# Optimization experiments

Hardware: AMD Instinct MI355X
Metric: run time of the kernel (lower is better)

Reference implementation:

```python
import jax, jax.numpy as jnp
import numpy as np

N = 100000   # nodes
E = 1600000  # edges (avg degree 16)
IN = 24
HID = 128
OUT = 12


def setup_inputs() -> dict:
    key = jax.random.key(0)
    ks = jax.random.split(key, 16)
    s = 0.05
    return {
        "inputs": jax.random.normal(ks[0], (N, IN), jnp.float32),
        "src": jax.random.randint(ks[1], (E,), 0, N),
        "dst": jax.random.randint(ks[2], (E,), 0, N),
        "e_w": jax.random.uniform(ks[3], (E, 1), jnp.float32),
        "snorm_n": jax.random.uniform(ks[4], (N, 1), jnp.float32),
        "snorm_e": jax.random.uniform(ks[5], (E, 1), jnp.float32),
        "W_emb": jax.random.normal(ks[6], (IN, HID), jnp.float32) * s,
        "b_emb": jnp.zeros((HID,), jnp.float32),
        "W_self1": jax.random.normal(ks[7], (HID, HID), jnp.float32) * s,
        "W1": jax.random.normal(ks[8], (HID, HID), jnp.float32) * s,
        "b1": jnp.zeros((HID,), jnp.float32),
        "W_self2": jax.random.normal(ks[9], (HID, HID), jnp.float32) * s,
        "W2": jax.random.normal(ks[10], (HID, HID), jnp.float32) * s,
        "b2": jnp.zeros((HID,), jnp.float32),
        "W_fc": jax.random.normal(ks[11], (HID, OUT), jnp.float32) * s,
        "b_fc": jnp.zeros((OUT,), jnp.float32),
    }


def _degrees(src, dst):
    out_deg = jnp.clip(jnp.zeros((N,), jnp.float32).at[src].add(1.0), 1.0)
    in_deg = jnp.clip(jnp.zeros((N,), jnp.float32).at[dst].add(1.0), 1.0)
    return out_deg, in_deg


def _gcn_layer(h, src, dst, e_w, out_deg, in_deg, W_self, W, b):
    # self transform (no bias)
    h_s = h @ W_self
    # source-side symmetric norm, edge-weighted message, sum-aggregate at dst
    feat = h * (out_deg ** -0.5)[:, None]          # [N, H]
    m = feat[src] * e_w                            # [E, H]  u_mul_e
    agg = jax.ops.segment_sum(m, dst, num_segments=N)  # [N, H] sum reduce
    h2 = (agg @ W + b) * (in_deg ** -0.5)[:, None]
    return h_s + h2


def reference(inputs, src, dst, e_w, snorm_n, snorm_e,
              W_emb, b_emb, W_self1, W1, b1, W_self2, W2, b2, W_fc, b_fc):
    out_deg, in_deg = _degrees(src, dst)
    h = inputs @ W_emb + b_emb
    h = jax.nn.relu(_gcn_layer(h, src, dst, e_w, out_deg, in_deg, W_self1, W1, b1))
    h = jax.nn.relu(_gcn_layer(h, src, dst, e_w, out_deg, in_deg, W_self2, W2, b2))
    return h @ W_fc + b_fc
```

## Files before the change

### kernel.cpp

```cpp
#include <hip/hip_runtime.h>

#define NN 100000
#define EE 1600000
#define IN_F 24
#define HID 128
#define OUT_F 12
#define HC 256
#define LBLK 128

#define DEG_WIN 16384
#define DEG_GRP 7
#define DEG_BPG 48
#define DEG_BLKS (DEG_GRP * DEG_BPG)

#define NBKT 782
#define PA_BLKS 512
#define PA_EPB 3125

#define EMB_B 2048
#define PREP_B 264
#define K1_GRID (DEG_BLKS + PA_BLKS + EMB_B + PREP_B)

typedef unsigned char u8;
typedef unsigned short u16;
typedef unsigned int u32;

using short8 = __attribute__((ext_vector_type(8))) short;
using f32x4  = __attribute__((ext_vector_type(4))) float;

__device__ __forceinline__ float bf2f(u16 h) {
  return __uint_as_float(((u32)h) << 16);
}
__device__ __forceinline__ u16 f2bf(float f) {
  u32 u = __float_as_uint(f);
  u32 r = (u + 0x7FFFu + ((u >> 16) & 1u)) >> 16;
  return (u16)r;
}
__device__ __forceinline__ float inv_sqrt_cnt(int c) {
  if (c < 1) c = 1;
  return 1.0f / sqrtf((float)c);
}

__device__ __forceinline__ void emb_body(int eb, const float* __restrict__ inputs,
                                         const float* __restrict__ W_emb,
                                         const float* __restrict__ b_emb,
                                         u16* __restrict__ hcat, float* smemW) {
  int t = threadIdx.x;
  float* Wls = smemW;
  float* bls = smemW + IN_F * HID;
  for (int i = t; i < IN_F * HID; i += 256) Wls[i] = W_emb[i];
  if (t < HID) bls[t] = b_emb[t];
  __syncthreads();
  int c = t & 127;
  int sub = t >> 7;
  for (int node = eb * 2 + sub; node < NN; node += EMB_B * 2) {
    const float* xr = inputs + (size_t)node * IN_F;
    float acc = bls[c];
    #pragma unroll
    for (int k = 0; k < IN_F; ++k) acc = fmaf(xr[k], Wls[k * HID + c], acc);
    hcat[(size_t)node * HC + c] = f2bf(acc);
  }
}

__device__ __forceinline__ void prep_body(int pb,
    const float* __restrict__ Ws1, const float* __restrict__ W1m,
    const float* __restrict__ Ws2, const float* __restrict__ W2m,
    const float* __restrict__ Wfc,
    u16* __restrict__ WT1, u16* __restrict__ WT2, u16* __restrict__ WfcT) {
  int idx = pb * 256 + (int)threadIdx.x;
  if (idx < 65536) {
    int layer = idx >> 15;
    int rem = idx & 32767;
    int n = rem >> 8, k = rem & 255;
    const float* A = layer ? Ws2 : Ws1;
    const float* B = layer ? W2m : W1m;
    float v = (k < HID) ? A[(size_t)k * HID + n] : B[(size_t)(k - HID) * HID + n];
    (layer ? WT2 : WT1)[(size_t)n * 256 + k] = f2bf(v);
  } else if (idx < 65536 + 2048) {
    int j = idx - 65536;
    int n = j >> 7, k = j & 127;
    WfcT[(size_t)n * 128 + k] = f2bf(n < OUT_F ? Wfc[(size_t)k * OUT_F + n] : 0.f);
  }
}

__global__ __launch_bounds__(256) void k1(
    const int* __restrict__ src, const int* __restrict__ dst,
    u16* __restrict__ whist, u32* __restrict__ histg,
    const float* __restrict__ inputs, const float* __restrict__ W_emb,
    const float* __restrict__ b_emb, u16* __restrict__ hcat,
    const float* __restrict__ Ws1, const float* __restrict__ W1m,
    const float* __restrict__ Ws2, const float* __restrict__ W2m,
    const float* __restrict__ Wfc,
    u16* __restrict__ WT1, u16* __restrict__ WT2, u16* __restrict__ WfcT) {
  __shared__ __align__(16) char sm_raw[65536];
  int b = blockIdx.x, t = threadIdx.x;
  if (b < DEG_BLKS) {
    u32* hist = (u32*)sm_raw;
    int g = b / DEG_BPG, sb = b % DEG_BPG;
    for (int i = t; i < DEG_WIN; i += 256) hist[i] = 0;
    __syncthreads();
    for (int e = sb * 256 + t; e < EE; e += DEG_BPG * 256) {
      int s = src[e];
      if ((s >> 14) == g) atomicAdd(&hist[s & (DEG_WIN - 1)], 1u);
    }
    __syncthreads();
    u16* wout = whist + (size_t)b * DEG_WIN;
    for (int i = t; i < DEG_WIN; i += 256) wout[i] = (u16)hist[i];
  } else if (b < DEG_BLKS + PA_BLKS) {
    u32* hist = (u32*)sm_raw;
    int pb = b - DEG_BLKS;
    for (int i = t; i < 1024; i += 256) hist[i] = 0;
    __syncthreads();
    int e0 = pb * PA_EPB;
    for (int e = e0 + t; e < e0 + PA_EPB; e += 256)
      atomicAdd(&hist[dst[e] >> 7], 1u);
    __syncthreads();
    for (int i = t; i < 1024; i += 256) histg[(size_t)pb * 1024 + i] = hist[i];
  } else if (b < DEG_BLKS + PA_BLKS + EMB_B) {
    emb_body(b - DEG_BLKS - PA_BLKS, inputs, W_emb, b_emb, hcat, (float*)sm_raw);
  } else {
    prep_body(b - DEG_BLKS - PA_BLKS - EMB_B, Ws1, W1m, Ws2, W2m, Wfc, WT1, WT2, WfcT);
  }
}

__global__ __launch_bounds__(256) void k2scan1(const u16* __restrict__ whist,
                                               float* __restrict__ out_norm,
                                               u32* __restrict__ histg,
                                               u32* __restrict__ totals) {
  __shared__ u32 s[512];
  int b = blockIdx.x, t = threadIdx.x;
  if (b < NBKT) {
    int k = b;
    u32 v0 = histg[(size_t)t * 1024 + k];
    u32 v1 = histg[(size_t)(t + 256) * 1024 + k];
    s[t] = v0; s[t + 256] = v1;
    __syncthreads();
    for (int off = 1; off < 512; off <<= 1) {
      u32 a0 = (t >= off) ? s[t - off] : 0;
      u32 a1 = (t + 256 >= off) ? s[t + 256 - off] : 0;
      __syncthreads();
      s[t] += a0; s[t + 256] += a1;
      __syncthreads();
    }
    histg[(size_t)t * 1024 + k] = s[t] - v0;
    histg[(size_t)(t + 256) * 1024 + k] = s[t + 256] - v1;
    if (t == 255) totals[k] = s[511];
  } else {
    int n = (b - NBKT) * 256 + t;
    if (n < NN) {
      int g = n >> 14, i = n & (DEG_WIN - 1);
      const u16* base = whist + ((size_t)g * DEG_BPG) * DEG_WIN + i;
      u32 sum = 0;
      #pragma unroll
      for (int bb = 0; bb < DEG_BPG; ++bb) sum += base[(size_t)bb * DEG_WIN];
      out_norm[n] = inv_sqrt_cnt((int)sum);
    }
  }
}

__global__ __launch_bounds__(1024) void k_scan2(const u32* __restrict__ totals,
                                                u32* __restrict__ estart) {
  __shared__ u32 s[1024];
  int t = threadIdx.x;
  u32 v = (t < NBKT) ? totals[t] : 0;
  s[t] = v;
  __syncthreads();
  for (int off = 1; off < 1024; off <<= 1) {
    u32 a = (t >= off) ? s[t - off] : 0;
    __syncthreads();
    s[t] += a;
    __syncthreads();
  }
  if (t < NBKT) estart[t] = s[t] - v;
  if (t == NBKT - 1) estart[NBKT] = s[t];
}

__global__ __launch_bounds__(256) void k_passb(
    const int* __restrict__ src, const int* __restrict__ dst,
    const float* __restrict__ e_w, const float* __restrict__ out_norm,
    const u32* __restrict__ histg, const u32* __restrict__ estart,
    u32* __restrict__ csr_stage, u8* __restrict__ dl8) {
  __shared__ u32 cur[1024];
  int pb = blockIdx.x, t = threadIdx.x;
  for (int i = t; i < 1024; i += 256)
    cur[i] = ((i < NBKT) ? estart[i] : 0u) + histg[(size_t)pb * 1024 + i];
  __syncthreads();
  int e0 = pb * PA_EPB;
  for (int e = e0 + t; e < e0 + PA_EPB; e += 256) {
    int s = src[e], d = dst[e];
    float w = e_w[e] * out_norm[s];
    u32 pos = atomicAdd(&cur[d >> 7], 1u);
    csr_stage[pos] = (((u32)f2bf(w)) << 17) | (u32)s;
    dl8[pos] = (u8)(d & 127);
  }
}

__global__ __launch_bounds__(256) void k_reorder(
    const u32* __restrict__ csr_stage, const u8* __restrict__ dl8,
    const u32* __restrict__ estart, u32* __restrict__ csr,
    int* __restrict__ row_start, float* __restrict__ in_norm) {
  __shared__ u32 cnt[128], pfx[128], cur[128];
  int k = blockIdx.x, t = threadIdx.x;
  if (t < 128) cnt[t] = 0;
  __syncthreads();
  int e0 = (int)estart[k], e1 = (int)estart[k + 1];
  for (int e = e0 + t; e < e1; e += 256) atomicAdd(&cnt[dl8[e]], 1u);
  __syncthreads();
  if (t < 128) pfx[t] = cnt[t];
  __syncthreads();
  for (int off = 1; off < 128; off <<= 1) {
    u32 v = (t < 128 && t >= off) ? pfx[t - off] : 0;
    __syncthreads();
    if (t < 128) pfx[t] += v;
    __syncthreads();
  }
  if (t < 128) {
    u32 start = (u32)e0 + pfx[t] - cnt[t];
    cur[t] = start;
    int node = k * 128 + t;
    if (node < NN) {
      row_start[node] = (int)start;
      in_norm[node] = inv_sqrt_cnt((int)cnt[t]);
    }
  }
  if (k == NBKT - 1 && t == 0) row_start[NN] = e1;
  __syncthreads();
  for (int e = e0 + t; e < e1; e += 256) {
    u32 pos = atomicAdd(&cur[dl8[e]], 1u);
    csr[pos] = csr_stage[e];
  }
}

__global__ __launch_bounds__(256) void k_agg(const u16* __restrict__ hcat_in,
                                             const int* __restrict__ row_start,
                                             const float* __restrict__ in_norm,
                                             const u32* __restrict__ csr,
                                             u16* __restrict__ hcat_out) {
  int t = threadIdx.x;
  int node = blockIdx.x * 8 + (t >> 5);
  if (node >= NN) return;
  int lane = t & 31;
  int s0 = row_start[node], s1 = row_start[node + 1];
  float ax = 0.f, ay = 0.f, az = 0.f, aw = 0.f;
  for (int i0 = s0; i0 < s1; i0 += 32) {
    u32 pk = 0;
    if (i0 + lane < s1) pk = csr[i0 + lane];
    int m = s1 - i0; if (m > 32) m = 32;
    for (int j = 0; j < m; ++j) {
      u32 p = __shfl(pk, j, 32);
      float w = bf2f((u16)(p >> 17));
      int sv = (int)(p & 0x1FFFF);
      ushort4 hv = *(const ushort4*)(hcat_in + (size_t)sv * HC + lane * 4);
      ax = fmaf(w, bf2f(hv.x), ax);
      ay = fmaf(w, bf2f(hv.y), ay);
      az = fmaf(w, bf2f(hv.z), az);
      aw = fmaf(w, bf2f(hv.w), aw);
    }
  }
  float inn = in_norm[node];
  ushort4 r;
  r.x = f2bf(ax * inn); r.y = f2bf(ay * inn);
  r.z = f2bf(az * inn); r.w = f2bf(aw * inn);
  *(ushort4*)(hcat_out + (size_t)node * HC + HID + lane * 4) = r;
}

template<int FC>
__global__ __launch_bounds__(512) void k_layer(u16* __restrict__ hcat,
    const u16* __restrict__ WT, const float* __restrict__ bias,
    const float* __restrict__ in_norm,
    const u16* __restrict__ WfcT, const float* __restrict__ b_fc,
    float* __restrict__ out) {
  __shared__ char smem[135168];
  const int t = threadIdx.x;
  const int r0 = blockIdx.x * LBLK;

  #pragma unroll
  for (int i = 0; i < 8; ++i) {
    int boff = i * 8192 + t * 16;
    int row = boff >> 9, col = boff & 511;
    uint4 v = *(const uint4*)(hcat + (size_t)(r0 + row) * HC + (col >> 1));
    *(uint4*)(smem + row * 512 + (col ^ ((row & 7) << 4))) = v;
  }
  #pragma unroll
  for (int i = 0; i < 8; ++i) {
    int boff = i * 8192 + t * 16;
    int row = boff >> 9, col = boff & 511;
    uint4 v = *(const uint4*)(WT + (size_t)row * 256 + (col >> 1));
    *(uint4*)(smem + 65536 + row * 512 + (col ^ ((row & 7) << 4))) = v;
  }
  if (FC && t < 256) {
    int row = t >> 4, col = (t & 15) * 16;
    uint4 v = *(const uint4*)(WfcT + (size_t)row * 128 + (col >> 1));
    *(uint4*)(smem + 131072 + row * 256 + (col ^ ((row & 7) << 4))) = v;
  }
  __syncthreads();

  const int lane = t & 63, w = t >> 6;
  const int l15 = lane & 15, lhi = lane >> 4;

  f32x4 acc[8];
  #pragma unroll
  for (int nf = 0; nf < 8; ++nf) acc[nf] = (f32x4){0.f, 0.f, 0.f, 0.f};

  const int arow = w * 16 + l15;
  const char* pa = smem + arow * 512;
  const int aswz = (arow & 7) << 4;
  #pragma unroll
  for (int ks = 0; ks < 8; ++ks) {
    int kb = ks * 64 + (lhi << 4);
    short8 a = *(const short8*)(pa + (kb ^ aswz));
    #pragma unroll
    for (int nf = 0; nf < 8; ++nf) {
      int brow = nf * 16 + l15;
      short8 bf = *(const short8*)(smem + 65536 + brow * 512 + (kb ^ ((brow & 7) << 4)));
      acc[nf] = __builtin_amdgcn_mfma_f32_16x16x32_bf16(a, bf, acc[nf], 0, 0, 0);
    }
  }

  float bcol[8];
  #pragma unroll
  for (int nf = 0; nf < 8; ++nf) bcol[nf] = bias[nf * 16 + l15];

  if (!FC) {
    #pragma unroll
    for (int r = 0; r < 4; ++r) {
      int grow = r0 + w * 16 + (lhi << 2) + r;
      if (grow < NN) {
        float inn = in_norm[grow];
        #pragma unroll
        for (int nf = 0; nf < 8; ++nf) {
          float v = acc[nf][r] + inn * bcol[nf];
          hcat[(size_t)grow * HC + nf * 16 + l15] = f2bf(fmaxf(v, 0.f));
        }
      }
    }
  } else {
    #pragma unroll
    for (int r = 0; r < 4; ++r) {
      int lrow = w * 16 + (lhi << 2) + r;
      int grow = r0 + lrow;
      float inn = (grow < NN) ? in_norm[grow] : 0.f;
      #pragma unroll
      for (int nf = 0; nf < 8; ++nf) {
        int col = nf * 16 + l15;
        float v = fmaxf(acc[nf][r] + inn * bcol[nf], 0.f);
        *(u16*)(smem + lrow * 256 + ((col * 2) ^ ((lrow & 7) << 4))) = f2bf(v);
      }
    }
    __syncthreads();
    f32x4 a2 = (f32x4){0.f, 0.f, 0.f, 0.f};
    const char* pa2 = smem + (w * 16 + l15) * 256;
    const int as2 = (l15 & 7) << 4;
    #pragma unroll
    for (int ks = 0; ks < 4; ++ks) {
      int kb = ks * 64 + (lhi << 4);
      short8 a = *(const short8*)(pa2 + (kb ^ as2));
      short8 bf = *(const short8*)(smem + 131072 + l15 * 256 + (kb ^ as2));
      a2 = __builtin_amdgcn_mfma_f32_16x16x32_bf16(a, bf, a2, 0, 0, 0);
    }
    if (l15 < OUT_F) {
      float bo = b_fc[l15];
      #pragma unroll
      for (int r = 0; r < 4; ++r) {
        int grow = r0 + w * 16 + (lhi << 2) + r;
        if (grow < NN) out[(size_t)grow * OUT_F + l15] = a2[r] + bo;
      }
    }
  }
}

extern "C" void kernel_launch(void* const* d_in, const int* in_sizes, int n_in,
                              void* d_out, int out_size, void* d_ws, size_t ws_size,
                              hipStream_t stream) {
  (void)in_sizes; (void)n_in; (void)out_size;
  const float* inputs  = (const float*)d_in[0];
  const int*   src     = (const int*)d_in[1];
  const int*   dst     = (const int*)d_in[2];
  const float* e_w     = (const float*)d_in[3];
  const float* W_emb   = (const float*)d_in[6];
  const float* b_emb   = (const float*)d_in[7];
  const float* W_self1 = (const float*)d_in[8];
  const float* W1      = (const float*)d_in[9];
  const float* b1      = (const float*)d_in[10];
  const float* W_self2 = (const float*)d_in[11];
  const float* W2      = (const float*)d_in[12];
  const float* b2      = (const float*)d_in[13];
  const float* W_fc    = (const float*)d_in[14];
  const float* b_fc    = (const float*)d_in[15];
  float* out = (float*)d_out;

  u32* histg       = (u32*)d_ws;
  u32* totals      = histg + (size_t)512 * 1024;
  u32* estart      = totals + 1024;
  float* out_norm  = (float*)(estart + 1024);
  float* in_norm   = out_norm + NN;
  int* row_start   = (int*)(in_norm + NN);
  u32* csr_stage   = (u32*)(row_start + NN + 4);
  u8* dl8          = (u8*)(csr_stage + EE);
  u32* csr         = (u32*)(dl8 + EE);
  u16* hcat        = (u16*)(csr + EE);
  u16* WT1         = hcat + (size_t)NN * HC;
  u16* WT2         = WT1 + 32768;
  u16* WfcT        = WT2 + 32768;
  u16* whist       = (u16*)csr_stage;

  const size_t NEED = (size_t)512 * 1024 * 4 + 2048 * 4 + (size_t)(3 * NN + 4) * 4
                      + (size_t)EE * 9 + (size_t)NN * HC * 2 + (2 * 32768 + 2048) * 2;
  if (ws_size < NEED) return;

  hipLaunchKernelGGL(k1, dim3(K1_GRID), dim3(256), 0, stream,
                     src, dst, whist, histg, inputs, W_emb, b_emb, hcat,
                     W_self1, W1, W_self2, W2, W_fc, WT1, WT2, WfcT);
  hipLaunchKernelGGL(k2scan1, dim3(NBKT + (NN + 255) / 256), dim3(256), 0, stream,
                     whist, out_norm, histg, totals);
  hipLaunchKernelGGL(k_scan2, dim3(1), dim3(1024), 0, stream, totals, estart);
  hipLaunchKernelGGL(k_passb, dim3(PA_BLKS), dim3(256), 0, stream,
                     src, dst, e_w, out_norm, histg, estart, csr_stage, dl8);
  hipLaunchKernelGGL(k_reorder, dim3(NBKT), dim3(256), 0, stream,
                     csr_stage, dl8, estart, csr, row_start, in_norm);
  hipLaunchKernelGGL(k_agg, dim3((NN + 7) / 8), dim3(256), 0, stream,
                     hcat, row_start, in_norm, csr, hcat);
  hipLaunchKernelGGL(k_layer<0>, dim3((NN + LBLK - 1) / LBLK), dim3(512), 0, stream,
                     hcat, WT1, b1, in_norm, WfcT, b_fc, out);
  hipLaunchKernelGGL(k_agg, dim3((NN + 7) / 8), dim3(256), 0, stream,
                     hcat, row_start, in_norm, csr, hcat);
  hipLaunchKernelGGL(k_layer<1>, dim3((NN + LBLK - 1) / LBLK), dim3(512), 0, stream,
                     hcat, WT2, b2, in_norm, WfcT, b_fc, out);
}
```

Before: 389.3 us.

## Compute out-degree via bucketed counting sort instead of windowed histograms

Replaces the 336-block windowed shared-memory histogram for source out-degrees, which read the whole src array 48 times per group, with a two-level bucket count. Src is counted alongside dst in k1, scanned, scattered into 128-node buckets of low-byte ids, then counted per bucket to produce out_norm. This cuts redundant src reads and frees 64KB of LDS in k1, at the cost of two extra kernel launches and an extra scatter pass over the edges. The lo8 buffer is reused for dl8 afterwards.

```diff
diff --git a/kernel.cpp b/kernel.cpp
--- a/kernel.cpp
+++ b/kernel.cpp
@@ -8,18 +8,13 @@
 #define HC 256
 #define LBLK 128
 
-#define DEG_WIN 16384
-#define DEG_GRP 7
-#define DEG_BPG 48
-#define DEG_BLKS (DEG_GRP * DEG_BPG)
-
 #define NBKT 782
 #define PA_BLKS 512
 #define PA_EPB 3125
 
 #define EMB_B 2048
 #define PREP_B 264
-#define K1_GRID (DEG_BLKS + PA_BLKS + EMB_B + PREP_B)
+#define K1_GRID (PA_BLKS + EMB_B + PREP_B)
 
 typedef unsigned char u8;
 typedef unsigned short u16;
@@ -85,84 +80,71 @@
 
 __global__ __launch_bounds__(256) void k1(
     const int* __restrict__ src, const int* __restrict__ dst,
-    u16* __restrict__ whist, u32* __restrict__ histg,
+    u32* __restrict__ histgD, u32* __restrict__ histgS,
     const float* __restrict__ inputs, const float* __restrict__ W_emb,
     const float* __restrict__ b_emb, u16* __restrict__ hcat,
     const float* __restrict__ Ws1, const float* __restrict__ W1m,
     const float* __restrict__ Ws2, const float* __restrict__ W2m,
     const float* __restrict__ Wfc,
     u16* __restrict__ WT1, u16* __restrict__ WT2, u16* __restrict__ WfcT) {
-  __shared__ __align__(16) char sm_raw[65536];
+  __shared__ __align__(16) char sm[13312];
   int b = blockIdx.x, t = threadIdx.x;
-  if (b < DEG_BLKS) {
-    u32* hist = (u32*)sm_raw;
-    int g = b / DEG_BPG, sb = b % DEG_BPG;
-    for (int i = t; i < DEG_WIN; i += 256) hist[i] = 0;
-    __syncthreads();
-    for (int e = sb * 256 + t; e < EE; e += DEG_BPG * 256) {
-      int s = src[e];
-      if ((s >> 14) == g) atomicAdd(&hist[s & (DEG_WIN - 1)], 1u);
-    }
-    __syncthreads();
-    u16* wout = whist + (size_t)b * DEG_WIN;
-    for (int i = t; i < DEG_WIN; i += 256) wout[i] = (u16)hist[i];
-  } else if (b < DEG_BLKS + PA_BLKS) {
-    u32* hist = (u32*)sm_raw;
-    int pb = b - DEG_BLKS;
-    for (int i = t; i < 1024; i += 256) hist[i] = 0;
-    __syncthreads();
-    int e0 = pb * PA_EPB;
-    for (int e = e0 + t; e < e0 + PA_EPB; e += 256)
-      atomicAdd(&hist[dst[e] >> 7], 1u);
-    __syncthreads();
-    for (int i = t; i < 1024; i += 256) histg[(size_t)pb * 1024 + i] = hist[i];
-  } else if (b < DEG_BLKS + PA_BLKS + EMB_B) {
-    emb_body(b - DEG_BLKS - PA_BLKS, inputs, W_emb, b_emb, hcat, (float*)sm_raw);
+  if (b < PA_BLKS) {
+    u32* histD = (u32*)sm;
+    u32* histS = histD + 1024;
+    for (int i = t; i < 2048; i += 256) histD[i] = 0;
+    __syncthreads();
+    int e0 = b * PA_EPB;
+    for (int e = e0 + t; e < e0 + PA_EPB; e += 256) {
+      atomicAdd(&histD[dst[e] >> 7], 1u);
+      atomicAdd(&histS[src[e] >> 7], 1u);
+    }
+    __syncthreads();
+    for (int i = t; i < 1024; i += 256) {
+      histgD[(size_t)b * 1024 + i] = histD[i];
+      histgS[(size_t)b * 1024 + i] = histS[i];
+    }
+  } else if (b < PA_BLKS + EMB_B) {
+    emb_body(b - PA_BLKS, inputs, W_emb, b_emb, hcat, (float*)sm);
   } else {
-    prep_body(b - DEG_BLKS - PA_BLKS - EMB_B, Ws1, W1m, Ws2, W2m, Wfc, WT1, WT2, WfcT);
-  }
-}
-
-__global__ __launch_bounds__(256) void k2scan1(const u16* __restrict__ whist,
-                                               float* __restrict__ out_norm,
-                                               u32* __restrict__ histg,
-                                               u32* __restrict__ totals) {
+    prep_body(b - PA_BLKS - EMB_B, Ws1, W1m, Ws2, W2m, Wfc, WT1, WT2, WfcT);
+  }
+}
+
+__global__ __launch_bounds__(256) void k_scan1(u32* __restrict__ histgD,
+                                               u32* __restrict__ histgS,
+                                               u32* __restrict__ totalsD,
+                                               u32* __restrict__ totalsS) {
   __shared__ u32 s[512];
   int b = blockIdx.x, t = threadIdx.x;
-  if (b < NBKT) {
-    int k = b;
-    u32 v0 = histg[(size_t)t * 1024 + k];
-    u32 v1 = histg[(size_t)(t + 256) * 1024 + k];
-    s[t] = v0; s[t + 256] = v1;
-    __syncthreads();
-    for (int off = 1; off < 512; off <<= 1) {
-      u32 a0 = (t >= off) ? s[t - off] : 0;
-      u32 a1 = (t + 256 >= off) ? s[t + 256 - off] : 0;
-      __syncthreads();
-      s[t] += a0; s[t + 256] += a1;
-      __syncthreads();
-    }
-    histg[(size_t)t * 1024 + k] = s[t] - v0;
-    histg[(size_t)(t + 256) * 1024 + k] = s[t + 256] - v1;
-    if (t == 255) totals[k] = s[511];
-  } else {
-    int n = (b - NBKT) * 256 + t;
-    if (n < NN) {
-      int g = n >> 14, i = n & (DEG_WIN - 1);
-      const u16* base = whist + ((size_t)g * DEG_BPG) * DEG_WIN + i;
-      u32 sum = 0;
-      #pragma unroll
-      for (int bb = 0; bb < DEG_BPG; ++bb) sum += base[(size_t)bb * DEG_WIN];
-      out_norm[n] = inv_sqrt_cnt((int)sum);
-    }
-  }
-}
-
-__global__ __launch_bounds__(1024) void k_scan2(const u32* __restrict__ totals,
-                                                u32* __restrict__ estart) {
+  u32* hist = (b < NBKT) ? histgD : histgS;
+  u32* tot  = (b < NBKT) ? totalsD : totalsS;
+  int k = (b < NBKT) ? b : b - NBKT;
+  u32 v0 = hist[(size_t)t * 1024 + k];
+  u32 v1 = hist[(size_t)(t + 256) * 1024 + k];
+  s[t] = v0; s[t + 256] = v1;
+  __syncthreads();
+  for (int off = 1; off < 512; off <<= 1) {
+    u32 a0 = (t >= off) ? s[t - off] : 0;
+    u32 a1 = (t + 256 >= off) ? s[t + 256 - off] : 0;
+    __syncthreads();
+    s[t] += a0; s[t + 256] += a1;
+    __syncthreads();
+  }
+  hist[(size_t)t * 1024 + k] = s[t] - v0;
+  hist[(size_t)(t + 256) * 1024 + k] = s[t + 256] - v1;
+  if (t == 255) tot[k] = s[511];
+}
+
+__global__ __launch_bounds__(1024) void k_scan2(const u32* __restrict__ totalsD,
+                                                const u32* __restrict__ totalsS,
+                                                u32* __restrict__ estartD,
+                                                u32* __restrict__ sstart) {
   __shared__ u32 s[1024];
+  const u32* tot = blockIdx.x ? totalsS : totalsD;
+  u32* est       = blockIdx.x ? sstart  : estartD;
   int t = threadIdx.x;
-  u32 v = (t < NBKT) ? totals[t] : 0;
+  u32 v = (t < NBKT) ? tot[t] : 0;
   s[t] = v;
   __syncthreads();
   for (int off = 1; off < 1024; off <<= 1) {
@@ -171,19 +153,51 @@
     s[t] += a;
     __syncthreads();
   }
-  if (t < NBKT) estart[t] = s[t] - v;
-  if (t == NBKT - 1) estart[NBKT] = s[t];
-}
-
-__global__ __launch_bounds__(256) void k_passb(
+  if (t < NBKT) est[t] = s[t] - v;
+  if (t == NBKT - 1) est[NBKT] = s[t];
+}
+
+__global__ __launch_bounds__(256) void k_passbS(
+    const int* __restrict__ src, const u32* __restrict__ histgS,
+    const u32* __restrict__ sstart, u8* __restrict__ lo8) {
+  __shared__ u32 cur[1024];
+  int pb = blockIdx.x, t = threadIdx.x;
+  for (int i = t; i < 1024; i += 256)
+    cur[i] = ((i < NBKT) ? sstart[i] : 0u) + histgS[(size_t)pb * 1024 + i];
+  __syncthreads();
+  int e0 = pb * PA_EPB;
+  for (int e = e0 + t; e < e0 + PA_EPB; e += 256) {
+    int s = src[e];
+    u32 pos = atomicAdd(&cur[s >> 7], 1u);
+    lo8[pos] = (u8)(s & 127);
+  }
+}
+
+__global__ __launch_bounds__(256) void k_countS(const u8* __restrict__ lo8,
+                                                const u32* __restrict__ sstart,
+                                                float* __restrict__ out_norm) {
+  __shared__ u32 cnt[128];
+  int k = blockIdx.x, t = threadIdx.x;
+  if (t < 128) cnt[t] = 0;
+  __syncthreads();
+  int e0 = (int)sstart[k], e1 = (int)sstart[k + 1];
+  for (int e = e0 + t; e < e1; e += 256) atomicAdd(&cnt[lo8[e]], 1u);
+  __syncthreads();
+  if (t < 128) {
+    int node = k * 128 + t;
+    if (node < NN) out_norm[node] = inv_sqrt_cnt((int)cnt[t]);
+  }
+}
+
+__global__ __launch_bounds__(256) void k_passbD(
     const int* __restrict__ src, const int* __restrict__ dst,
     const float* __restrict__ e_w, const float* __restrict__ out_norm,
-    const u32* __restrict__ histg, const u32* __restrict__ estart,
+    const u32* __restrict__ histgD, const u32* __restrict__ estartD,
     u32* __restrict__ csr_stage, u8* __restrict__ dl8) {
   __shared__ u32 cur[1024];
   int pb = blockIdx.x, t = threadIdx.x;
   for (int i = t; i < 1024; i += 256)
-    cur[i] = ((i < NBKT) ? estart[i] : 0u) + histg[(size_t)pb * 1024 + i];
+    cur[i] = ((i < NBKT) ? estartD[i] : 0u) + histgD[(size_t)pb * 1024 + i];
   __syncthreads();
   int e0 = pb * PA_EPB;
   for (int e = e0 + t; e < e0 + PA_EPB; e += 256) {
@@ -389,35 +403,41 @@
   const float* b_fc    = (const float*)d_in[15];
   float* out = (float*)d_out;
 
-  u32* histg       = (u32*)d_ws;
-  u32* totals      = histg + (size_t)512 * 1024;
-  u32* estart      = totals + 1024;
-  float* out_norm  = (float*)(estart + 1024);
+  u32* histgD      = (u32*)d_ws;
+  u32* histgS      = histgD + (size_t)512 * 1024;
+  u32* totalsD     = histgS + (size_t)512 * 1024;
+  u32* estartD     = totalsD + 1024;
+  u32* totalsS     = estartD + 1024;
+  u32* sstart      = totalsS + 1024;
+  float* out_norm  = (float*)(sstart + 1024);
   float* in_norm   = out_norm + NN;
   int* row_start   = (int*)(in_norm + NN);
-  u32* csr_stage   = (u32*)(row_start + NN + 4);
-  u8* dl8          = (u8*)(csr_stage + EE);
-  u32* csr         = (u32*)(dl8 + EE);
+  u8* lo8          = (u8*)(row_start + NN + 4);
+  u32* csr_stage   = (u32*)(lo8 + EE);
+  u32* csr         = csr_stage + EE;
   u16* hcat        = (u16*)(csr + EE);
   u16* WT1         = hcat + (size_t)NN * HC;
   u16* WT2         = WT1 + 32768;
   u16* WfcT        = WT2 + 32768;
-  u16* whist       = (u16*)csr_stage;
-
-  const size_t NEED = (size_t)512 * 1024 * 4 + 2048 * 4 + (size_t)(3 * NN + 4) * 4
+
+  const size_t NEED = (size_t)2 * 512 * 1024 * 4 + 4096 * 4 + (size_t)(3 * NN + 4) * 4
                       + (size_t)EE * 9 + (size_t)NN * HC * 2 + (2 * 32768 + 2048) * 2;
   if (ws_size < NEED) return;
 
   hipLaunchKernelGGL(k1, dim3(K1_GRID), dim3(256), 0, stream,
-                     src, dst, whist, histg, inputs, W_emb, b_emb, hcat,
+                     src, dst, histgD, histgS, inputs, W_emb, b_emb, hcat,
                      W_self1, W1, W_self2, W2, W_fc, WT1, WT2, WfcT);
-  hipLaunchKernelGGL(k2scan1, dim3(NBKT + (NN + 255) / 256), dim3(256), 0, stream,
-                     whist, out_norm, histg, totals);
-  hipLaunchKernelGGL(k_scan2, dim3(1), dim3(1024), 0, stream, totals, estart);
-  hipLaunchKernelGGL(k_passb, dim3(PA_BLKS), dim3(256), 0, stream,
-                     src, dst, e_w, out_norm, histg, estart, csr_stage, dl8);
+  hipLaunchKernelGGL(k_scan1, dim3(2 * NBKT), dim3(256), 0, stream,
+                     histgD, histgS, totalsD, totalsS);
+  hipLaunchKernelGGL(k_scan2, dim3(2), dim3(1024), 0, stream,
+                     totalsD, totalsS, estartD, sstart);
+  hipLaunchKernelGGL(k_passbS, dim3(PA_BLKS), dim3(256), 0, stream,
+                     src, histgS, sstart, lo8);
+  hipLaunchKernelGGL(k_countS, dim3(NBKT), dim3(256), 0, stream, lo8, sstart, out_norm);
+  hipLaunchKernelGGL(k_passbD, dim3(PA_BLKS), dim3(256), 0, stream,
+                     src, dst, e_w, out_norm, histgD, estartD, csr_stage, lo8);
   hipLaunchKernelGGL(k_reorder, dim3(NBKT), dim3(256), 0, stream,
-                     csr_stage, dl8, estart, csr, row_start, in_norm);
+                     csr_stage, lo8, estartD, csr, row_start, in_norm);
   hipLaunchKernelGGL(k_agg, dim3((NN + 7) / 8), dim3(256), 0, stream,
                      hcat, row_start, in_norm, csr, hcat);
   hipLaunchKernelGGL(k_layer<0>, dim3((NN + LBLK - 1) / LBLK), dim3(512), 0, stream,
```

Result: faster. 381.0 us (-2.1%).
